# Kernel optimization log

Hardware: AMD Instinct MI355X
Metric: run time of the kernel (lower is better)

Reference implementation:

```python
import jax, jax.numpy as jnp
import numpy as np

# --- static config (forward defaults of InstanSeg_Torchscript.forward) ---
H = W = 512
K = 256          # max instances (top-K local maxima, padded with validity mask)
WS = 32          # window_size -> slice_size = 2*WS
S = 2 * WS
PD = 5           # peak_distance (neighbourhood for local max)
SEED_T = 0.7     # seed_threshold
MASK_T = 0.53    # mask_threshold
MIN_SIZE = 10.0  # min object area
MEAN_T = 0.0     # mean mask-value threshold
OVL_T = 0.3      # overlap (IoU) threshold for merging
CC_ITERS = 32    # label-propagation iterations for connected components


def setup_inputs() -> dict:
    key = jax.random.key(0)
    k1, k2, k3 = jax.random.split(key, 3)
    x = jax.random.normal(k1, (1, 5, H, W), jnp.float32)  # backbone output: 2 fields + 2 sigma + 1 seed
    w_cls = jax.random.normal(k2, (4,), jnp.float32)      # pixel classifier over (dy,dx,sig0,sig1)
    b_cls = jax.random.normal(k3, (1,), jnp.float32)
    return {"x": x, "w_cls": w_cls, "b_cls": b_cls}


def _windows_and_probs(x, w_cls, b_cls):
    """Peak-local-max seed detection + per-instance windowed classification."""
    feat = x[0]                                           # [5,H,W]
    yy, xx = jnp.meshgrid(jnp.arange(H, dtype=jnp.float32),
                          jnp.arange(W, dtype=jnp.float32), indexing='ij')
    coords = jnp.stack([yy, xx])                          # [2,H,W] coordinate map
    fields = feat[0:2] + coords                           # spatial embedding fields
    sigma = feat[2:4]
    mask_map = jax.nn.sigmoid(feat[4])

    # torch_peak_local_max: local maxima in (2*PD+1) window above seed_threshold
    pool = jax.lax.reduce_window(mask_map, -jnp.inf, jax.lax.max,
                                 (2 * PD + 1, 2 * PD + 1), (1, 1), 'SAME')
    peak_score = jnp.where((mask_map == pool) & (mask_map > SEED_T), mask_map, -1.0)
    vals, idx = jax.lax.top_k(peak_score.reshape(-1), K)
    valid = vals > SEED_T                                 # [K]
    cy, cx = idx // W, idx % W
    c = jnp.stack([cy, cx], axis=1).astype(jnp.float32)   # to_centre=True: coords at centroids

    # clamp window centres so the SxS window fits inside the image
    wy = jnp.clip(cy, WS, H - WS)
    wx = jnp.clip(cx, WS, W - WS)
    offs = jnp.arange(S)
    gy = (wy - WS)[:, None, None] + offs[None, :, None]   # [K,S,S]
    gx = (wx - WS)[:, None, None] + offs[None, None, :]   # [K,S,S]

    fw = fields[:, gy, gx]                                # [2,K,S,S] gathered field windows
    sw = sigma[:, gy, gx]                                 # [2,K,S,S]
    d = fw - c.T[:, :, None, None]                        # field offset to own centroid
    f = jnp.concatenate([d, sw], axis=0)                  # [4,K,S,S] engineered features
    probs = jax.nn.sigmoid(jnp.einsum('f,fkij->kij', w_cls, f) + b_cls[0])  # [K,S,S]
    probs = probs * valid[:, None, None]                  # zero out padded instances
    return probs, gy, gx, mask_map, valid


def reference(x, w_cls, b_cls):
    probs, gy, gx, mask_map, valid = _windows_and_probs(x, w_cls, b_cls)
    HW = H * W
    fidx = gy * W + gx                                    # [K,S,S] flat image index per window pixel
    mask = probs > MASK_T

    # convert(): per-pixel winner = instance with max prob above threshold (scatter-max)
    maxp = jnp.zeros((HW,), probs.dtype).at[fidx].max(jnp.where(mask, probs, 0.0))
    winners = mask & (probs >= maxp[fidx])
    ids = (jnp.arange(K, dtype=jnp.int32) + 1)[:, None, None]
    lab = jnp.zeros((HW,), jnp.int32).at[fidx].max(jnp.where(winners, ids, 0))

    # sparse one-hot [K, H*W] (dense here; K=256 keeps it ~268MB)
    iK = jnp.arange(K)[:, None, None]
    onehot = jnp.zeros((K, HW), jnp.float32).at[iK, fidx].max(mask.astype(jnp.float32))
    areas = onehot.sum(axis=1)
    mean_val = (onehot @ mask_map.reshape(-1)) / jnp.maximum(areas, 1.0)
    remove = ~((mean_val > MEAN_T) & (areas > MIN_SIZE)) | ~valid

    # fast_sparse_iou + find_connected_components: merge overlapping instances
    inter = onehot @ onehot.T                             # [K,K]
    union = areas[:, None] + areas[None, :] - inter
    adj = (inter / jnp.maximum(union, 1.0)) > OVL_T       # symmetric, diag True

    def body(_, lbl):
        return jnp.min(jnp.where(adj, lbl[None, :], K), axis=1)
    lbl = jax.lax.fori_loop(0, CC_ITERS, body, jnp.arange(K))  # min-label propagation

    # remap_values + drop removed objects
    roots = jnp.where(lab > 0, lbl[jnp.clip(lab - 1, 0, K - 1)] + 1, 0)
    rm = remove[jnp.clip(roots - 1, 0, K - 1)]
    final = jnp.where((roots > 0) & ~rm, roots, 0)
    labels = final.reshape(1, 1, H, W).astype(jnp.float32)
    return labels, probs
```

## Files before the change

### kernel.cpp

```cpp
#include <hip/hip_runtime.h>
#include <stdint.h>

#define HH   512
#define WWI  512
#define HWN  (HH*WWI)
#define KK   256
#define WSR  32
#define SSW  64
#define RPB  4
#define HALO 5
#define SROWS (RPB + 2*HALO)
#define NFRONT 128
#define CPB  32
#define CAND_CAP 4096
#define SUB  4

#define OFF_PACKED 0u
#define OFF_BITSG  2097152u
#define OFF_AREA   3145728u
#define OFF_MSUM   3146752u
#define OFF_WY0    3147776u
#define OFF_WX0    3148800u
#define OFF_ADJ    3149824u
#define OFF_CAND   3158016u
#define OFF_RANK   3190784u
#define OFF_CNT    3207168u

__device__ __forceinline__ float sigm(float v) {
    return 1.0f / (1.0f + expf(-v));
}

__global__ __launch_bounds__(256) void k_front(const float* __restrict__ x4,
        unsigned long long* __restrict__ cand,
        unsigned long long* __restrict__ packed,
        unsigned long long* __restrict__ bitsG,
        float* __restrict__ areas, float* __restrict__ msum,
        int* __restrict__ iy0, int* __restrict__ ix0,
        int* __restrict__ rankbuf, int* __restrict__ cnt) {
    int tid = threadIdx.x, bid = blockIdx.x;
    if (bid < NFRONT) {
        __shared__ float vm[RPB][WWI];
        __shared__ int lcnt;
        int r0 = bid * RPB;
        if (tid == 0) lcnt = 0;
        if (tid < CPB) cand[bid * CPB + tid] = 0ull;
        float s0[SROWS], s1[SROWS];
        #pragma unroll
        for (int hr = 0; hr < SROWS; ++hr) {
            int gr = r0 - HALO + hr; gr = gr < 0 ? 0 : (gr > HH-1 ? HH-1 : gr);
            const float* row = x4 + gr * WWI;
            s0[hr] = sigm(row[tid]);
            s1[hr] = sigm(row[tid + 256]);
        }
        #pragma unroll
        for (int rr = 0; rr < RPB; ++rr) {
            float a = s0[rr], b = s1[rr];
            #pragma unroll
            for (int d = 1; d < 11; ++d) { a = fmaxf(a, s0[rr+d]); b = fmaxf(b, s1[rr+d]); }
            vm[rr][tid] = a; vm[rr][tid + 256] = b;
        }
        __syncthreads();
        #pragma unroll
        for (int rr = 0; rr < RPB; ++rr) {
            int gy = r0 + rr;
            {
                int c = tid;
                float m = s0[rr + HALO];
                if (m > 0.7f) {
                    int c0 = c-5 < 0 ? 0 : c-5, c1 = c+5;
                    float v = -1.0f;
                    for (int cc = c0; cc <= c1; ++cc) v = fmaxf(v, vm[rr][cc]);
                    if (m == v) {
                        int slot = atomicAdd(&lcnt, 1);
                        if (slot < CPB) {
                            unsigned p = (unsigned)(gy * WWI + c);
                            cand[bid * CPB + slot] =
                                ((unsigned long long)__float_as_uint(m) << 32) |
                                (unsigned long long)(0xFFFFFFFFu - p);
                        }
                    }
                }
            }
            {
                int c = tid + 256;
                float m = s1[rr + HALO];
                if (m > 0.7f) {
                    int c0 = c-5, c1 = c+5 > 511 ? 511 : c+5;
                    float v = -1.0f;
                    for (int cc = c0; cc <= c1; ++cc) v = fmaxf(v, vm[rr][cc]);
                    if (m == v) {
                        int slot = atomicAdd(&lcnt, 1);
                        if (slot < CPB) {
                            unsigned p = (unsigned)(gy * WWI + c);
                            cand[bid * CPB + slot] =
                                ((unsigned long long)__float_as_uint(m) << 32) |
                                (unsigned long long)(0xFFFFFFFFu - p);
                        }
                    }
                }
            }
        }
    } else {
        int gt = (bid - NFRONT) * 256 + tid;
        ulonglong2 z; z.x = 0ull; z.y = 0ull;
        ulonglong2* p2 = (ulonglong2*)(packed + (size_t)gt * 8);
        p2[0] = z; p2[1] = z; p2[2] = z; p2[3] = z;
        ulonglong2* b2 = (ulonglong2*)(bitsG + (size_t)gt * 4);
        b2[0] = z; b2[1] = z;
        if (gt < CAND_CAP) rankbuf[gt] = 0;
        if (gt < KK) { areas[gt] = 0.0f; msum[gt] = 0.0f; iy0[gt] = 0; ix0[gt] = 0; }
        if (gt == 0) *cnt = 0;
    }
}

__global__ __launch_bounds__(256) void k_rank(const unsigned long long* __restrict__ cand,
                                              int* __restrict__ rankbuf,
                                              int* __restrict__ cnt) {
    __shared__ unsigned long long kl[256];
    int tid = threadIdx.x;
    int bx = blockIdx.x & 15, by = blockIdx.x >> 4;
    int ibase = bx * 256, jbase = by * 256;
    kl[tid] = cand[jbase + tid];
    unsigned long long my = cand[ibase + tid];
    if (by == 0) {
        unsigned long long bal = __ballot(my != 0ull);
        if ((tid & 63) == 0) atomicAdd(cnt, (int)__popcll(bal));
    }
    __syncthreads();
    if (my == 0ull) return;
    int r0 = 0, r1 = 0, r2 = 0, r3 = 0, r4 = 0, r5 = 0, r6 = 0, r7 = 0;
    #pragma unroll 4
    for (int j = 0; j < 256; j += 8) {
        unsigned long long a0 = kl[j+0], a1 = kl[j+1], a2 = kl[j+2], a3 = kl[j+3];
        unsigned long long a4 = kl[j+4], a5 = kl[j+5], a6 = kl[j+6], a7 = kl[j+7];
        r0 += (a0 > my); r1 += (a1 > my); r2 += (a2 > my); r3 += (a3 > my);
        r4 += (a4 > my); r5 += (a5 > my); r6 += (a6 > my); r7 += (a7 > my);
    }
    int r = (r0 + r1) + (r2 + r3) + ((r4 + r5) + (r6 + r7));
    if (r) atomicAdd(&rankbuf[ibase + tid], r);
}

__global__ __launch_bounds__(256) void k_win2(const float* __restrict__ x,
        const float* __restrict__ wc, const float* __restrict__ bc,
        const unsigned long long* __restrict__ cand,
        const int* __restrict__ rankbuf, const int* __restrict__ cnt,
        float* __restrict__ probs, unsigned long long* __restrict__ packed,
        unsigned long long* __restrict__ bitsG,
        float* __restrict__ areas, float* __restrict__ msum,
        int* __restrict__ iy0, int* __restrict__ ix0) {
    int bid = blockIdx.x, tid = threadIdx.x;
    int lane = tid & 63;
    if (bid >= SUB * CAND_CAP) {
        int j = bid - SUB * CAND_CAP;
        int c = *cnt; if (c > KK) c = KK;
        if (j >= c) for (int i = tid; i < 4096; i += 256) probs[j * 4096 + i] = 0.0f;
        return;
    }
    int c = bid >> 2, sub = bid & 3;
    unsigned long long my = cand[c];
    if (my == 0ull) return;
    int k = rankbuf[c];
    if (k >= KK) return;

    unsigned pp = 0xFFFFFFFFu - (unsigned)(my & 0xFFFFFFFFull);
    int cy = (int)(pp >> 9), cx = (int)(pp & 511);
    int wy = cy < WSR ? WSR : (cy > HH - WSR ? HH - WSR : cy);
    int wx = cx < WSR ? WSR : (cx > WWI - WSR ? WWI - WSR : cx);
    int gy0 = wy - WSR, gx0 = wx - WSR;
    if (sub == 0 && tid == 0) { iy0[k] = gy0; ix0[k] = gx0; }

    __shared__ float sA, sM;
    if (tid == 0) { sA = 0.0f; sM = 0.0f; }
    __syncthreads();
    float w0 = wc[0], w1 = wc[1], w2 = wc[2], w3 = wc[3], b = bc[0];
    float cyf = (float)cy, cxf = (float)cx;
    const float* x0 = x;
    const float* x1 = x + HWN;
    const float* x2 = x + 2 * HWN;
    const float* x3 = x + 3 * HWN;
    const float* x4 = x + 4 * HWN;
    unsigned long long idbits = (unsigned long long)(unsigned)(k + 1);
    float aA = 0.0f, aM = 0.0f;
    #pragma unroll
    for (int q = 0; q < 4; ++q) {
        int p = (((sub << 2) + q) << 8) + tid;
        int row = p >> 6;
        int col = p & 63;
        int gy = gy0 + row, gx = gx0 + col;
        int g = gy * WWI + gx;
        float gyf = (float)gy;
        float d0 = __fsub_rn(__fadd_rn(x0[g], gyf), cyf);
        float d1 = __fsub_rn(__fadd_rn(x1[g], (float)gx), cxf);
        float s0v = x2[g], s1v = x3[g];
        float t = __fadd_rn(
                    __fadd_rn(
                      __fadd_rn(
                        __fadd_rn(__fmul_rn(w0, d0), __fmul_rn(w1, d1)),
                        __fmul_rn(w2, s0v)),
                      __fmul_rn(w3, s1v)),
                    b);
        float pr = sigm(t);
        probs[k * 4096 + p] = pr;
        bool pass = pr > 0.53f;
        unsigned long long bal = __ballot(pass);
        if (lane == 0) bitsG[(size_t)gy * 256 + k] = bal;
        if (pass) {
            aA += 1.0f;
            aM += sigm(x4[g]);
            atomicMax(&packed[g],
                      ((unsigned long long)__float_as_uint(pr) << 32) | idbits);
        }
    }
    #pragma unroll
    for (int off = 32; off; off >>= 1) {
        aA += __shfl_down(aA, off);
        aM += __shfl_down(aM, off);
    }
    if (lane == 0) { atomicAdd(&sA, aA); atomicAdd(&sM, aM); }
    __syncthreads();
    if (tid == 0) { atomicAdd(&areas[k], sA); atomicAdd(&msum[k], sM); }
}

__global__ __launch_bounds__(256) void k_pairs(
        const unsigned long long* __restrict__ bitsG,
        const float* __restrict__ areas,
        const int* __restrict__ iy0, const int* __restrict__ ix0,
        unsigned long long* __restrict__ adj) {
    int a = blockIdx.x, tid = threadIdx.x;
    int b2 = tid;
    int ay0 = iy0[a], ax0 = ix0[a];
    int bx0 = ix0[b2];
    int xl = max(ax0, bx0), xh = min(ax0 + SSW, bx0 + SSW);
    int inter = 0;
    if (xl < xh) {
        int wdt = xh - xl;
        unsigned long long cmask = (wdt >= 64) ? ~0ull : ((1ull << wdt) - 1ull);
        int sa = xl - ax0, sb = xl - bx0;
        for (int i = 0; i < SSW; ++i) {
            int gy = ay0 + i;
            unsigned long long wa = bitsG[(size_t)gy * 256 + a];
            unsigned long long wb = bitsG[(size_t)gy * 256 + b2];
            inter += __popcll((wa >> sa) & (wb >> sb) & cmask);
        }
    }
    float fi = (float)inter;
    float uni = __fsub_rn(__fadd_rn(areas[a], areas[b2]), fi);
    bool adjb = (fi / fmaxf(uni, 1.0f)) > 0.3f;
    unsigned long long bal = __ballot(adjb);
    if ((tid & 63) == 0) adj[a * 4 + (tid >> 6)] = bal;
}

__global__ __launch_bounds__(256) void k_final(
        const unsigned long long* __restrict__ packed,
        const int* __restrict__ cnt,
        const unsigned long long* __restrict__ adj,
        const float* __restrict__ areas, const float* __restrict__ msum,
        float* __restrict__ labels) {
    __shared__ unsigned long long adjS[KK][4];
    __shared__ int lbl[KK];
    __shared__ int fmS[KK];
    __shared__ unsigned char rem[KK];
    __shared__ int changed;
    int tid = threadIdx.x;
    for (int w = 0; w < 4; ++w) adjS[tid][w] = adj[tid * 4 + w];
    lbl[tid] = tid;
    __syncthreads();
    int cntv = *cnt;
    for (int it = 0; it < 32; ++it) {
        int m = KK;
        for (int w = 0; w < 4; ++w) {
            unsigned long long bb = adjS[tid][w];
            while (bb) {
                int j = __ffsll((unsigned long long)bb) - 1;
                int v = lbl[(w << 6) | j];
                m = v < m ? v : m;
                bb &= bb - 1;
            }
        }
        if (tid == 0) changed = 0;
        __syncthreads();
        if (m != lbl[tid]) { lbl[tid] = m; atomicOr(&changed, 1); }
        __syncthreads();
        if (!changed) break;
    }
    float area = areas[tid];
    bool validf = tid < cntv;
    float mean = msum[tid] / fmaxf(area, 1.0f);
    rem[tid] = (unsigned char)(!((mean > 0.0f) && (area > 10.0f) && validf));
    __syncthreads();
    {
        int root = lbl[tid];
        int rc = root < 255 ? root : 255;
        fmS[tid] = rem[rc] ? 0 : (root + 1);
    }
    __syncthreads();

    int i = blockIdx.x * 256 + tid;
    const ulonglong2* p2 = (const ulonglong2*)(packed + (size_t)i * 4);
    ulonglong2 a = p2[0], b = p2[1];
    float4 o;
    unsigned l0 = (unsigned)(a.x & 0xFFFFFFFFull);
    unsigned l1 = (unsigned)(a.y & 0xFFFFFFFFull);
    unsigned l2 = (unsigned)(b.x & 0xFFFFFFFFull);
    unsigned l3 = (unsigned)(b.y & 0xFFFFFFFFull);
    o.x = l0 ? (float)fmS[l0 - 1] : 0.0f;
    o.y = l1 ? (float)fmS[l1 - 1] : 0.0f;
    o.z = l2 ? (float)fmS[l2 - 1] : 0.0f;
    o.w = l3 ? (float)fmS[l3 - 1] : 0.0f;
    *(float4*)(labels + (size_t)i * 4) = o;
}

extern "C" void kernel_launch(void* const* d_in, const int* in_sizes, int n_in,
                              void* d_out, int out_size, void* d_ws, size_t ws_size,
                              hipStream_t stream) {
    const float* x  = (const float*)d_in[0];
    const float* wc = (const float*)d_in[1];
    const float* bc = (const float*)d_in[2];
    float* labels = (float*)d_out;
    float* probs  = (float*)d_out + HWN;

    char* ws = (char*)d_ws;
    unsigned long long* packed  = (unsigned long long*)(ws + OFF_PACKED);
    unsigned long long* bitsG   = (unsigned long long*)(ws + OFF_BITSG);
    float*              areas   = (float*)(ws + OFF_AREA);
    float*              msum    = (float*)(ws + OFF_MSUM);
    int*                iy0p    = (int*)(ws + OFF_WY0);
    int*                ix0p    = (int*)(ws + OFF_WX0);
    unsigned long long* adj     = (unsigned long long*)(ws + OFF_ADJ);
    unsigned long long* cand    = (unsigned long long*)(ws + OFF_CAND);
    int*                rankbuf = (int*)(ws + OFF_RANK);
    int*                cnt     = (int*)(ws + OFF_CNT);

    k_front<<<256, 256, 0, stream>>>(x + 4 * HWN, cand, packed, bitsG,
                                     areas, msum, iy0p, ix0p, rankbuf, cnt);
    k_rank <<<256, 256, 0, stream>>>(cand, rankbuf, cnt);
    k_win2 <<<SUB * CAND_CAP + KK, 256, 0, stream>>>(x, wc, bc, cand, rankbuf, cnt,
                                                     probs, packed, bitsG,
                                                     areas, msum, iy0p, ix0p);
    k_pairs<<<KK, 256, 0, stream>>>(bitsG, areas, iy0p, ix0p, adj);
    k_final<<<HWN / 1024, 256, 0, stream>>>(packed, cnt, adj, areas, msum, labels);
}
```

Baseline: 46.32 us.

## Compact ranked seeds into winner list and launch window kernel per instance

Adds a small compaction kernel that scatters each top-K candidate's index into a winners array by rank. The window kernel then launches SUB*K blocks instead of SUB*CAND_CAP+K, so thousands of early-exit blocks for empty or low-ranked candidates disappear. Each instance's window is also split over 8 sub-blocks instead of 4 for more parallelism per instance. Empty slots zero their probs slice with float4 stores. The cost is one extra kernel launch and a dependency on the winners buffer.

```diff
diff --git a/kernel.cpp b/kernel.cpp
--- a/kernel.cpp
+++ b/kernel.cpp
@@ -13,7 +13,7 @@
 #define NFRONT 128
 #define CPB  32
 #define CAND_CAP 4096
-#define SUB  4
+#define SUB  8
 
 #define OFF_PACKED 0u
 #define OFF_BITSG  2097152u
@@ -24,7 +24,8 @@
 #define OFF_ADJ    3149824u
 #define OFF_CAND   3158016u
 #define OFF_RANK   3190784u
-#define OFF_CNT    3207168u
+#define OFF_WIN    3207168u
+#define OFF_CNT    3208192u
 
 __device__ __forceinline__ float sigm(float v) {
     return 1.0f / (1.0f + expf(-v));
@@ -36,7 +37,8 @@
         unsigned long long* __restrict__ bitsG,
         float* __restrict__ areas, float* __restrict__ msum,
         int* __restrict__ iy0, int* __restrict__ ix0,
-        int* __restrict__ rankbuf, int* __restrict__ cnt) {
+        int* __restrict__ rankbuf, int* __restrict__ winners,
+        int* __restrict__ cnt) {
     int tid = threadIdx.x, bid = blockIdx.x;
     if (bid < NFRONT) {
         __shared__ float vm[RPB][WWI];
@@ -108,7 +110,8 @@
         ulonglong2* b2 = (ulonglong2*)(bitsG + (size_t)gt * 4);
         b2[0] = z; b2[1] = z;
         if (gt < CAND_CAP) rankbuf[gt] = 0;
-        if (gt < KK) { areas[gt] = 0.0f; msum[gt] = 0.0f; iy0[gt] = 0; ix0[gt] = 0; }
+        if (gt < KK) { areas[gt] = 0.0f; msum[gt] = 0.0f; iy0[gt] = 0; ix0[gt] = 0;
+                       winners[gt] = -1; }
         if (gt == 0) *cnt = 0;
     }
 }
@@ -140,28 +143,36 @@
     if (r) atomicAdd(&rankbuf[ibase + tid], r);
 }
 
+__global__ __launch_bounds__(256) void k_compact(
+        const unsigned long long* __restrict__ cand,
+        const int* __restrict__ rankbuf, int* __restrict__ winners) {
+    int c = blockIdx.x * 256 + threadIdx.x;
+    if (cand[c] != 0ull) {
+        int r = rankbuf[c];
+        if (r < KK) winners[r] = c;
+    }
+}
+
 __global__ __launch_bounds__(256) void k_win2(const float* __restrict__ x,
         const float* __restrict__ wc, const float* __restrict__ bc,
         const unsigned long long* __restrict__ cand,
-        const int* __restrict__ rankbuf, const int* __restrict__ cnt,
+        const int* __restrict__ winners,
         float* __restrict__ probs, unsigned long long* __restrict__ packed,
         unsigned long long* __restrict__ bitsG,
         float* __restrict__ areas, float* __restrict__ msum,
         int* __restrict__ iy0, int* __restrict__ ix0) {
     int bid = blockIdx.x, tid = threadIdx.x;
+    int k = bid >> 3, sub = bid & 7;
     int lane = tid & 63;
-    if (bid >= SUB * CAND_CAP) {
-        int j = bid - SUB * CAND_CAP;
-        int c = *cnt; if (c > KK) c = KK;
-        if (j >= c) for (int i = tid; i < 4096; i += 256) probs[j * 4096 + i] = 0.0f;
+    int c = winners[k];
+    if (c < 0) {
+        if (tid < 128) {
+            float4 z; z.x = 0.0f; z.y = 0.0f; z.z = 0.0f; z.w = 0.0f;
+            ((float4*)(probs + (size_t)k * 4096 + sub * 512))[tid] = z;
+        }
         return;
     }
-    int c = bid >> 2, sub = bid & 3;
     unsigned long long my = cand[c];
-    if (my == 0ull) return;
-    int k = rankbuf[c];
-    if (k >= KK) return;
-
     unsigned pp = 0xFFFFFFFFu - (unsigned)(my & 0xFFFFFFFFull);
     int cy = (int)(pp >> 9), cx = (int)(pp & 511);
     int wy = cy < WSR ? WSR : (cy > HH - WSR ? HH - WSR : cy);
@@ -182,8 +193,8 @@
     unsigned long long idbits = (unsigned long long)(unsigned)(k + 1);
     float aA = 0.0f, aM = 0.0f;
     #pragma unroll
-    for (int q = 0; q < 4; ++q) {
-        int p = (((sub << 2) + q) << 8) + tid;
+    for (int q = 0; q < 2; ++q) {
+        int p = (((sub << 1) + q) << 8) + tid;
         int row = p >> 6;
         int col = p & 63;
         int gy = gy0 + row, gx = gx0 + col;
@@ -200,7 +211,7 @@
                       __fmul_rn(w3, s1v)),
                     b);
         float pr = sigm(t);
-        probs[k * 4096 + p] = pr;
+        probs[(size_t)k * 4096 + p] = pr;
         bool pass = pr > 0.53f;
         unsigned long long bal = __ballot(pass);
         if (lane == 0) bitsG[(size_t)gy * 256 + k] = bal;
@@ -329,14 +340,17 @@
     unsigned long long* adj     = (unsigned long long*)(ws + OFF_ADJ);
     unsigned long long* cand    = (unsigned long long*)(ws + OFF_CAND);
     int*                rankbuf = (int*)(ws + OFF_RANK);
+    int*                winners = (int*)(ws + OFF_WIN);
     int*                cnt     = (int*)(ws + OFF_CNT);
 
-    k_front<<<256, 256, 0, stream>>>(x + 4 * HWN, cand, packed, bitsG,
-                                     areas, msum, iy0p, ix0p, rankbuf, cnt);
-    k_rank <<<256, 256, 0, stream>>>(cand, rankbuf, cnt);
-    k_win2 <<<SUB * CAND_CAP + KK, 256, 0, stream>>>(x, wc, bc, cand, rankbuf, cnt,
-                                                     probs, packed, bitsG,
-                                                     areas, msum, iy0p, ix0p);
-    k_pairs<<<KK, 256, 0, stream>>>(bitsG, areas, iy0p, ix0p, adj);
-    k_final<<<HWN / 1024, 256, 0, stream>>>(packed, cnt, adj, areas, msum, labels);
-}
+    k_front  <<<256, 256, 0, stream>>>(x + 4 * HWN, cand, packed, bitsG,
+                                       areas, msum, iy0p, ix0p, rankbuf,
+                                       winners, cnt);
+    k_rank   <<<256, 256, 0, stream>>>(cand, rankbuf, cnt);
+    k_compact<<<CAND_CAP / 256, 256, 0, stream>>>(cand, rankbuf, winners);
+    k_win2   <<<SUB * KK, 256, 0, stream>>>(x, wc, bc, cand, winners,
+                                            probs, packed, bitsG,
+                                            areas, msum, iy0p, ix0p);
+    k_pairs  <<<KK, 256, 0, stream>>>(bitsG, areas, iy0p, ix0p, adj);
+    k_final  <<<HWN / 1024, 256, 0, stream>>>(packed, cnt, adj, areas, msum, labels);
+}
```

Result: slower. 47.47 us (+2.5%).

## Fold candidate ranking and count into window kernel, drop k_rank launch

Applied to the files above, without the earlier changes.

Removes the separate k_rank kernel and the rankbuf and cnt clears. Each window block now computes its candidate's rank by scanning all 4096 candidates and doing a block reduction. The tail blocks recompute the valid-candidate count, and one of them writes cnt for k_final. This saves a kernel launch and its global atomics, but every live block repeats an O(CAND_CAP) scan of cand, and each candidate's rank is computed four times (once per sub-block).

```diff
diff --git a/kernel.cpp b/kernel.cpp
--- a/kernel.cpp
+++ b/kernel.cpp
@@ -23,8 +23,7 @@
 #define OFF_WX0    3148800u
 #define OFF_ADJ    3149824u
 #define OFF_CAND   3158016u
-#define OFF_RANK   3190784u
-#define OFF_CNT    3207168u
+#define OFF_CNT    3190784u
 
 __device__ __forceinline__ float sigm(float v) {
     return 1.0f / (1.0f + expf(-v));
@@ -35,8 +34,7 @@
         unsigned long long* __restrict__ packed,
         unsigned long long* __restrict__ bitsG,
         float* __restrict__ areas, float* __restrict__ msum,
-        int* __restrict__ iy0, int* __restrict__ ix0,
-        int* __restrict__ rankbuf, int* __restrict__ cnt) {
+        int* __restrict__ iy0, int* __restrict__ ix0) {
     int tid = threadIdx.x, bid = blockIdx.x;
     if (bid < NFRONT) {
         __shared__ float vm[RPB][WWI];
@@ -107,59 +105,47 @@
         p2[0] = z; p2[1] = z; p2[2] = z; p2[3] = z;
         ulonglong2* b2 = (ulonglong2*)(bitsG + (size_t)gt * 4);
         b2[0] = z; b2[1] = z;
-        if (gt < CAND_CAP) rankbuf[gt] = 0;
         if (gt < KK) { areas[gt] = 0.0f; msum[gt] = 0.0f; iy0[gt] = 0; ix0[gt] = 0; }
-        if (gt == 0) *cnt = 0;
-    }
-}
-
-__global__ __launch_bounds__(256) void k_rank(const unsigned long long* __restrict__ cand,
-                                              int* __restrict__ rankbuf,
-                                              int* __restrict__ cnt) {
-    __shared__ unsigned long long kl[256];
-    int tid = threadIdx.x;
-    int bx = blockIdx.x & 15, by = blockIdx.x >> 4;
-    int ibase = bx * 256, jbase = by * 256;
-    kl[tid] = cand[jbase + tid];
-    unsigned long long my = cand[ibase + tid];
-    if (by == 0) {
-        unsigned long long bal = __ballot(my != 0ull);
-        if ((tid & 63) == 0) atomicAdd(cnt, (int)__popcll(bal));
-    }
-    __syncthreads();
-    if (my == 0ull) return;
-    int r0 = 0, r1 = 0, r2 = 0, r3 = 0, r4 = 0, r5 = 0, r6 = 0, r7 = 0;
-    #pragma unroll 4
-    for (int j = 0; j < 256; j += 8) {
-        unsigned long long a0 = kl[j+0], a1 = kl[j+1], a2 = kl[j+2], a3 = kl[j+3];
-        unsigned long long a4 = kl[j+4], a5 = kl[j+5], a6 = kl[j+6], a7 = kl[j+7];
-        r0 += (a0 > my); r1 += (a1 > my); r2 += (a2 > my); r3 += (a3 > my);
-        r4 += (a4 > my); r5 += (a5 > my); r6 += (a6 > my); r7 += (a7 > my);
-    }
-    int r = (r0 + r1) + (r2 + r3) + ((r4 + r5) + (r6 + r7));
-    if (r) atomicAdd(&rankbuf[ibase + tid], r);
+    }
 }
 
 __global__ __launch_bounds__(256) void k_win2(const float* __restrict__ x,
         const float* __restrict__ wc, const float* __restrict__ bc,
         const unsigned long long* __restrict__ cand,
-        const int* __restrict__ rankbuf, const int* __restrict__ cnt,
         float* __restrict__ probs, unsigned long long* __restrict__ packed,
         unsigned long long* __restrict__ bitsG,
         float* __restrict__ areas, float* __restrict__ msum,
-        int* __restrict__ iy0, int* __restrict__ ix0) {
+        int* __restrict__ iy0, int* __restrict__ ix0,
+        int* __restrict__ cnt) {
     int bid = blockIdx.x, tid = threadIdx.x;
-    int lane = tid & 63;
+    int lane = tid & 63, wid = tid >> 6;
+    __shared__ int redI[4];
+    __shared__ float sA, sM;
     if (bid >= SUB * CAND_CAP) {
         int j = bid - SUB * CAND_CAP;
-        int c = *cnt; if (c > KK) c = KK;
-        if (j >= c) for (int i = tid; i < 4096; i += 256) probs[j * 4096 + i] = 0.0f;
+        int local = 0;
+        for (int i = tid; i < CAND_CAP; i += 256) local += (cand[i] != 0ull);
+        #pragma unroll
+        for (int off = 32; off; off >>= 1) local += __shfl_down(local, off);
+        if (lane == 0) redI[wid] = local;
+        __syncthreads();
+        int cntv = redI[0] + redI[1] + redI[2] + redI[3];
+        if (j == 0 && tid == 0) *cnt = cntv;
+        int cc = cntv < KK ? cntv : KK;
+        if (j >= cc) for (int i = tid; i < 4096; i += 256) probs[(size_t)j * 4096 + i] = 0.0f;
         return;
     }
     int c = bid >> 2, sub = bid & 3;
     unsigned long long my = cand[c];
     if (my == 0ull) return;
-    int k = rankbuf[c];
+    int local = 0;
+    for (int i = tid; i < CAND_CAP; i += 256) local += (cand[i] > my);
+    #pragma unroll
+    for (int off = 32; off; off >>= 1) local += __shfl_down(local, off);
+    if (tid == 0) { sA = 0.0f; sM = 0.0f; }
+    if (lane == 0) redI[wid] = local;
+    __syncthreads();
+    int k = redI[0] + redI[1] + redI[2] + redI[3];
     if (k >= KK) return;
 
     unsigned pp = 0xFFFFFFFFu - (unsigned)(my & 0xFFFFFFFFull);
@@ -169,9 +155,6 @@
     int gy0 = wy - WSR, gx0 = wx - WSR;
     if (sub == 0 && tid == 0) { iy0[k] = gy0; ix0[k] = gx0; }
 
-    __shared__ float sA, sM;
-    if (tid == 0) { sA = 0.0f; sM = 0.0f; }
-    __syncthreads();
     float w0 = wc[0], w1 = wc[1], w2 = wc[2], w3 = wc[3], b = bc[0];
     float cyf = (float)cy, cxf = (float)cx;
     const float* x0 = x;
@@ -200,7 +183,7 @@
                       __fmul_rn(w3, s1v)),
                     b);
         float pr = sigm(t);
-        probs[k * 4096 + p] = pr;
+        probs[(size_t)k * 4096 + p] = pr;
         bool pass = pr > 0.53f;
         unsigned long long bal = __ballot(pass);
         if (lane == 0) bitsG[(size_t)gy * 256 + k] = bal;
@@ -328,15 +311,13 @@
     int*                ix0p    = (int*)(ws + OFF_WX0);
     unsigned long long* adj     = (unsigned long long*)(ws + OFF_ADJ);
     unsigned long long* cand    = (unsigned long long*)(ws + OFF_CAND);
-    int*                rankbuf = (int*)(ws + OFF_RANK);
     int*                cnt     = (int*)(ws + OFF_CNT);
 
     k_front<<<256, 256, 0, stream>>>(x + 4 * HWN, cand, packed, bitsG,
-                                     areas, msum, iy0p, ix0p, rankbuf, cnt);
-    k_rank <<<256, 256, 0, stream>>>(cand, rankbuf, cnt);
-    k_win2 <<<SUB * CAND_CAP + KK, 256, 0, stream>>>(x, wc, bc, cand, rankbuf, cnt,
+                                     areas, msum, iy0p, ix0p);
+    k_win2 <<<SUB * CAND_CAP + KK, 256, 0, stream>>>(x, wc, bc, cand,
                                                      probs, packed, bitsG,
-                                                     areas, msum, iy0p, ix0p);
+                                                     areas, msum, iy0p, ix0p, cnt);
     k_pairs<<<KK, 256, 0, stream>>>(bitsG, areas, iy0p, ix0p, adj);
     k_final<<<HWN / 1024, 256, 0, stream>>>(packed, cnt, adj, areas, msum, labels);
 }
```

Measured after the change: 63.50 us. +37.1%, slower.
